# Kernel optimization log

Measured on AMD Instinct MI355X. Metric: run time of the kernel, lower is better.

Reference implementation:

```python
import jax, jax.numpy as jnp
import numpy as np

N, D = 128, 512  # batch, hypercube dim (in_features == n_2d_layers == out_features)

def setup_inputs() -> dict:
    key = jax.random.key(0)
    k1, k2, k3 = jax.random.split(key, 3)
    bound = 1.0 / np.sqrt(D)
    x = jax.random.normal(k1, (N, D, D), dtype=jnp.float32)
    # kaiming_uniform_(a=sqrt(5)) on (in, layers, out) ~ U(-1/sqrt(fan_in), 1/sqrt(fan_in)) scale
    w = jax.random.uniform(k2, (D, D, D), dtype=jnp.float32, minval=-bound, maxval=bound)
    b = jax.random.uniform(k3, (D, D), dtype=jnp.float32, minval=-bound, maxval=bound)
    return {"x": x, "w": w, "b": b}

def reference(x, w, b):
    # Original: (x.expand((L, *x.shape)).movedim(0,-2) * w).sum(-1) + b
    # which reduces to out[n,i,j] = sum_k x[n,i,k] * w[i,j,k] + b[i,j]
    # (w axes: (in_features, n_2d_layers, out_features), all equal D)
    return jnp.einsum('nik,ijk->nij', x, w) + b
```

## Files before the change

kernel.cpp:

```cpp
#include <hip/hip_runtime.h>


#define Dd 512
#define DD (512 * 512)
#define CHUNK 16
#define NCHUNK 32

typedef __attribute__((ext_vector_type(8))) short bf16x8;
typedef __attribute__((ext_vector_type(4))) short bf16x4;
typedef __attribute__((ext_vector_type(4))) float f32x4;

__device__ __forceinline__ short f2bf(float f) {
    unsigned u = __builtin_bit_cast(unsigned, f);
    u += 0x7FFFu + ((u >> 16) & 1u);
    return (short)(u >> 16);
}

__device__ __forceinline__ bf16x8 cvt8(float4 a, float4 b) {
    bf16x8 h;
    h[0] = f2bf(a.x); h[1] = f2bf(a.y); h[2] = f2bf(a.z); h[3] = f2bf(a.w);
    h[4] = f2bf(b.x); h[5] = f2bf(b.y); h[6] = f2bf(b.z); h[7] = f2bf(b.w);
    return h;
}

__device__ __forceinline__ void glds16(const float* g, float* l) {
    __builtin_amdgcn_global_load_lds(
        (const __attribute__((address_space(1))) void*)g,
        (__attribute__((address_space(3))) void*)l, 16, 0, 0);
}

__global__ __launch_bounds__(512, 4)
void linear3d_kernel(const float* __restrict__ x,
                     const float* __restrict__ w,
                     const float* __restrict__ b,
                     float* __restrict__ out) {
    const int i    = blockIdx.x;
    const int tid  = threadIdx.x;
    const int lane = tid & 63;
    const int wid  = tid >> 6;
    const int row16 = lane & 15;
    const int cg    = lane >> 4;

    __shared__ float f32s[CHUNK * Dd];
    __shared__ short b16[2][CHUNK * Dd];
    __shared__ float ldsb[Dd];

    const float* xi = x + (size_t)i * Dd;
    const float* wi = w + (size_t)i * DD;

    ldsb[tid] = b[i * Dd + tid];

    #pragma unroll
    for (int q = 0; q < 4; ++q)
        glds16(wi + (size_t)(wid * 256 + q * 64 + lane) * 4,
               &f32s[(wid * 256 + q * 64) * 4]);

    bf16x8 xf[16];
    {
        char* ws = (char*)&b16[0][0] + wid * 4096;
        #pragma unroll
        for (int r = 0; r < 16; ++r) {
            const float* xr = xi + (size_t)(wid * 16 + r) * DD;
            float4 va = *(const float4*)(xr + lane * 8);
            float4 vb = *(const float4*)(xr + lane * 8 + 4);
            char* slot = ws + (r & 3) * 1024;
            bf16x8 hv = cvt8(va, vb);
            *(bf16x8*)(slot + lane * 16) = hv;
            if (row16 == r) {
                #pragma unroll
                for (int s = 0; s < 16; ++s)
                    xf[s] = *(const bf16x8*)(slot + s * 64 + cg * 16);
            }
        }
    }

    __syncthreads();

    #pragma unroll
    for (int p = 0; p < 4; ++p) {
        int idx4 = tid + p * 512;
        int row = idx4 >> 7, c4 = idx4 & 127;
        float4 v = *(const float4*)(f32s + idx4 * 4);
        bf16x4 h = { f2bf(v.x), f2bf(v.y), f2bf(v.z), f2bf(v.w) };
        int byte = (row * 1024 + c4 * 8) ^ ((row & 7) << 4);
        *(bf16x4*)((char*)&b16[0][0] + byte) = h;
    }
    asm volatile("s_waitcnt lgkmcnt(0)" ::: "memory");
    __builtin_amdgcn_s_barrier();

    #pragma unroll
    for (int q = 0; q < 4; ++q)
        glds16(wi + (size_t)(CHUNK * Dd) + (size_t)(wid * 256 + q * 64 + lane) * 4,
               &f32s[(wid * 256 + q * 64) * 4]);

    const int nb = wid * 16;
    float* outbase = out + (size_t)i * Dd;

    for (int c = 0; c < NCHUNK; ++c) {
        const char* buf = (const char*)&b16[c & 1][0];
        f32x4 acc = {0.f, 0.f, 0.f, 0.f};
        #pragma unroll
        for (int s = 0; s < 16; ++s) {
            int byte = (row16 * 1024 + s * 64 + cg * 16) ^ ((row16 & 7) << 4);
            bf16x8 wf = *(const bf16x8*)(buf + byte);
            acc = __builtin_amdgcn_mfma_f32_16x16x32_bf16(xf[s], wf, acc, 0, 0, 0);
        }
        float bias = ldsb[c * 16 + row16];
        #pragma unroll
        for (int r = 0; r < 4; ++r) {
            int n = nb + cg * 4 + r;
            outbase[(size_t)n * DD + c * CHUNK + row16] = acc[r] + bias;
        }

        if (c + 1 < NCHUNK) {
            asm volatile("s_waitcnt lgkmcnt(0) vmcnt(4)" ::: "memory");
            __builtin_amdgcn_s_barrier();

            char* dstb = (char*)&b16[(c + 1) & 1][0];
            #pragma unroll
            for (int p = 0; p < 4; ++p) {
                int idx4 = tid + p * 512;
                int row = idx4 >> 7, cu = idx4 & 127;
                float4 v = *(const float4*)(f32s + idx4 * 4);
                bf16x4 h = { f2bf(v.x), f2bf(v.y), f2bf(v.z), f2bf(v.w) };
                int byte = (row * 1024 + cu * 8) ^ ((row & 7) << 4);
                *(bf16x4*)(dstb + byte) = h;
            }
            asm volatile("s_waitcnt lgkmcnt(0)" ::: "memory");
            __builtin_amdgcn_s_barrier();

            if (c + 2 < NCHUNK) {
                const float* src = wi + (size_t)(c + 2) * (CHUNK * Dd);
                #pragma unroll
                for (int q = 0; q < 4; ++q)
                    glds16(src + (size_t)(wid * 256 + q * 64 + lane) * 4,
                           &f32s[(wid * 256 + q * 64) * 4]);
            }
        }
    }
}

extern "C" void kernel_launch(void* const* d_in, const int* in_sizes, int n_in,
                              void* d_out, int out_size, void* d_ws, size_t ws_size,
                              hipStream_t stream) {
    const float* x = (const float*)d_in[0];
    const float* w = (const float*)d_in[1];
    const float* b = (const float*)d_in[2];
    float* out = (float*)d_out;
    linear3d_kernel<<<dim3(Dd), dim3(512), 0, stream>>>(x, w, b, out);
}
```

Before: 191.0 us.

## Swizzle block order, stage x rows cooperatively, use nontemporal output stores

Remaps block index so consecutive blocks handle strided i values, which changes how blocks spread across XCDs and their L2 caches. It also replaces the per-warp x load (each wave converting 16 rows independently) with 8 block-wide rounds that convert 16 rows at a time into swizzled LDS, then one wave pulls its fragments. Output writes become nontemporal stores to avoid polluting cache. The x staging adds 16 barriers and serializes fragment extraction, which could add latency in the prologue.

```diff
diff --git a/kernel.cpp b/kernel.cpp
--- a/kernel.cpp
+++ b/kernel.cpp
@@ -16,13 +16,6 @@
     return (short)(u >> 16);
 }
 
-__device__ __forceinline__ bf16x8 cvt8(float4 a, float4 b) {
-    bf16x8 h;
-    h[0] = f2bf(a.x); h[1] = f2bf(a.y); h[2] = f2bf(a.z); h[3] = f2bf(a.w);
-    h[4] = f2bf(b.x); h[5] = f2bf(b.y); h[6] = f2bf(b.z); h[7] = f2bf(b.w);
-    return h;
-}
-
 __device__ __forceinline__ void glds16(const float* g, float* l) {
     __builtin_amdgcn_global_load_lds(
         (const __attribute__((address_space(1))) void*)g,
@@ -34,7 +27,7 @@
                      const float* __restrict__ w,
                      const float* __restrict__ b,
                      float* __restrict__ out) {
-    const int i    = blockIdx.x;
+    const int i    = (blockIdx.x & 7) * 64 + (blockIdx.x >> 3);
     const int tid  = threadIdx.x;
     const int lane = tid & 63;
     const int wid  = tid >> 6;
@@ -55,25 +48,28 @@
         glds16(wi + (size_t)(wid * 256 + q * 64 + lane) * 4,
                &f32s[(wid * 256 + q * 64) * 4]);
 
+    short* xs = &b16[0][0];
     bf16x8 xf[16];
-    {
-        char* ws = (char*)&b16[0][0] + wid * 4096;
+    for (int r = 0; r < 8; ++r) {
+        __syncthreads();
         #pragma unroll
-        for (int r = 0; r < 16; ++r) {
-            const float* xr = xi + (size_t)(wid * 16 + r) * DD;
-            float4 va = *(const float4*)(xr + lane * 8);
-            float4 vb = *(const float4*)(xr + lane * 8 + 4);
-            char* slot = ws + (r & 3) * 1024;
-            bf16x8 hv = cvt8(va, vb);
-            *(bf16x8*)(slot + lane * 16) = hv;
-            if (row16 == r) {
-                #pragma unroll
-                for (int s = 0; s < 16; ++s)
-                    xf[s] = *(const bf16x8*)(slot + s * 64 + cg * 16);
+        for (int p = 0; p < 4; ++p) {
+            int idx4 = tid + p * 512;
+            int row = idx4 >> 7, c4 = idx4 & 127;
+            float4 v = *(const float4*)(xi + (size_t)(r * 16 + row) * DD + c4 * 4);
+            bf16x4 h = { f2bf(v.x), f2bf(v.y), f2bf(v.z), f2bf(v.w) };
+            int byte = (row * 1024 + c4 * 8) ^ ((row & 7) << 4);
+            *(bf16x4*)((char*)xs + byte) = h;
+        }
+        __syncthreads();
+        if (wid == r) {
+            #pragma unroll
+            for (int s = 0; s < 16; ++s) {
+                int byte = (row16 * 1024 + s * 64 + cg * 16) ^ ((row16 & 7) << 4);
+                xf[s] = *(const bf16x8*)((const char*)xs + byte);
             }
         }
     }
-
     __syncthreads();
 
     #pragma unroll
@@ -109,7 +105,8 @@
         #pragma unroll
         for (int r = 0; r < 4; ++r) {
             int n = nb + cg * 4 + r;
-            outbase[(size_t)n * DD + c * CHUNK + row16] = acc[r] + bias;
+            __builtin_nontemporal_store(acc[r] + bias,
+                outbase + (size_t)n * DD + c * CHUNK + row16);
         }
 
         if (c + 1 < NCHUNK) {
```

Result: slower. 209.3 us (+9.6%).
